# Kernel tuning notes

Hardware: AMD Instinct MI355X
Metric: run time of the kernel (lower is better)

The kernel has to match this reference:

```python
import jax, jax.numpy as jnp
import numpy as np

N, F_IN, H, E, G = 100000, 128, 64, 1600000, 256
BN_EPS = 1e-5


def setup_inputs() -> dict:
    key = jax.random.key(0)
    ks = jax.random.split(key, 32)
    rn = lambda k, shp, s=0.1: jax.random.normal(k, shp, jnp.float32) * s
    ru = lambda k, shp: jax.random.uniform(k, shp, jnp.float32)
    inp = {
        'x': jax.random.normal(ks[0], (N, F_IN), jnp.float32),
        'edge_index': jax.random.randint(ks[1], (2, E), 0, N),
        'batch': jnp.sort(jax.random.randint(ks[2], (N,), 0, G)),
        'w0': rn(ks[3], (F_IN, H)), 'b0': rn(ks[4], (H,)),
        'w1': rn(ks[5], (H, H)), 'b1': rn(ks[6], (H,)),
        'w2': rn(ks[7], (H, H)), 'b2': rn(ks[8], (H,)),
        'g0': ru(ks[9], (H,)) + 0.5, 'beta0': rn(ks[10], (H,)),
        'm0': rn(ks[11], (H,)), 'v0': ru(ks[12], (H,)) + 0.5,
        'g1': ru(ks[13], (H,)) + 0.5, 'beta1': rn(ks[14], (H,)),
        'm1': rn(ks[15], (H,)), 'v1': ru(ks[16], (H,)) + 0.5,
        'g2': ru(ks[17], (H,)) + 0.5, 'beta2': rn(ks[18], (H,)),
        'm2': rn(ks[19], (H,)), 'v2': ru(ks[20], (H,)) + 0.5,
        'l1w': rn(ks[21], (H, H // 2)), 'l1b': rn(ks[22], (H // 2,)),
        'l2w': rn(ks[23], (H // 2, 2)), 'l2b': rn(ks[24], (2,)),
    }
    return inp


def reference(x, edge_index, batch, w0, b0, w1, b1, w2, b2,
              g0, beta0, m0, v0, g1, beta1, m1, v1, g2, beta2, m2, v2,
              l1w, l1b, l2w, l2b):
    n = x.shape[0]
    # GCN: add self-loops, symmetric normalization deg^{-1/2} A_hat deg^{-1/2}
    loop = jnp.arange(n)
    src = jnp.concatenate([edge_index[0], loop])
    dst = jnp.concatenate([edge_index[1], loop])
    deg = jax.ops.segment_sum(jnp.ones_like(src, dtype=x.dtype), dst, num_segments=n)
    dinv = jax.lax.rsqrt(jnp.maximum(deg, 1.0))  # deg >= 1 after self-loops
    norm = (dinv[src] * dinv[dst])[:, None]      # [E+N, 1]

    def gcn(h, w, b):
        h = h @ w                                              # [N, H]
        agg = jax.ops.segment_sum(h[src] * norm, dst, num_segments=n)
        return agg + b

    def bn(h, g, be, m, v):  # eval-mode BatchNorm1d (running stats)
        return (h - m) * (g * jax.lax.rsqrt(v + BN_EPS)) + be

    h = jax.nn.relu(bn(gcn(x, w0, b0), g0, beta0, m0, v0))
    h = jax.nn.relu(bn(gcn(h, w1, b1), g1, beta1, m1, v1))
    h = jax.nn.relu(bn(gcn(h, w2, b2), g2, beta2, m2, v2))
    pooled = jax.ops.segment_sum(h, batch, num_segments=G)     # global_add_pool
    h = jax.nn.relu(pooled @ l1w + l1b)
    return h @ l2w + l2b                                        # [G, 2]
```

## Files before the change

### kernel.cpp

```cpp
#include <hip/hip_runtime.h>
#include <hip/hip_bf16.h>

#define BN_EPS 1e-5f

typedef short bf16x8 __attribute__((ext_vector_type(8)));
typedef float f32x4 __attribute__((ext_vector_type(4)));

static __device__ __forceinline__ unsigned short f2bf(float f) {
    unsigned u = __float_as_uint(f);
    unsigned r = (u + 0x7FFF + ((u >> 16) & 1)) >> 16;
    return (unsigned short)r;
}
static __device__ __forceinline__ float bf2f(unsigned short s) {
    return __uint_as_float((unsigned)s << 16);
}
__device__ __forceinline__ int pad4i(int c) { return (c + 3) & ~3; }

#define BIN_SHIFT 9
#define BIN_NODES 512
#define P1_CHUNK 8192
#define P1_THREADS 1024
#define P1_PER_THREAD (P1_CHUNK / P1_THREADS)
#define IMG_CAP 12288
#define P2_THREADS 512

__global__ __launch_bounds__(P1_THREADS) void phase1_kernel(
        const int* __restrict__ src, const int* __restrict__ dst,
        int* __restrict__ bincur, int* __restrict__ ebuf, int e, int ecap) {
    __shared__ int hist[256], base[256], cur[256];
    int t = threadIdx.x;
    int c0 = blockIdx.x * P1_CHUNK;
    int iend = c0 + P1_CHUNK; if (iend > e) iend = e;
    if (t < 256) hist[t] = 0;
    __syncthreads();
    int dreg[P1_PER_THREAD];
#pragma unroll
    for (int u = 0; u < P1_PER_THREAD; u++) {
        int i = c0 + t + u * P1_THREADS;
        if (i < iend) {
            int d = dst[i];
            dreg[u] = d;
            atomicAdd(&hist[d >> BIN_SHIFT], 1);
        }
    }
    __syncthreads();
    if (t < 256) {
        if (hist[t] > 0)
            base[t] = t * ecap + atomicAdd(&bincur[t], hist[t]);
        cur[t] = 0;
    }
    __syncthreads();
#pragma unroll
    for (int u = 0; u < P1_PER_THREAD; u++) {
        int i = c0 + t + u * P1_THREADS;
        if (i < iend) {
            int s = src[i], d = dreg[u];
            int b = d >> BIN_SHIFT;
            int r = atomicAdd(&cur[b], 1);
            int p = base[b] + r;
            if (p < (b + 1) * ecap)
                ebuf[p] = s | ((d & (BIN_NODES - 1)) << 17);
        }
    }
}

__global__ __launch_bounds__(1024) void bincount_kernel(
        const int* __restrict__ ebuf, const int* __restrict__ bincur, int ecap,
        float* __restrict__ dinv, int* __restrict__ row_start,
        int* __restrict__ row_len, int* __restrict__ binbase,
        int* __restrict__ binpad, int* __restrict__ gtotal,
        unsigned short* __restrict__ ha_sent, int n) {
    __shared__ int c512[BIN_NODES];
    __shared__ int sd[256];
    __shared__ int rbs;
    int b = blockIdx.x, t = threadIdx.x;
    if (b == 0 && t < 64) ha_sent[t] = 0;
    if (t < BIN_NODES) c512[t] = 0;
    __syncthreads();
    int cnt_b = bincur[b]; if (cnt_b > ecap) cnt_b = ecap;
    int e0 = b * ecap, e1 = e0 + cnt_b;
    for (int j = e0 + t; j < e1; j += 1024)
        atomicAdd(&c512[ebuf[j] >> 17], 1);
    __syncthreads();
    int n0 = b * BIN_NODES;
    if (t < BIN_NODES) {
        int i = n0 + t;
        if (i < n) dinv[i] = rsqrtf((float)(c512[t] + 1));
    }
    int v0 = 0, v1 = 0, tsum = 0;
    if (t < 256) {
        v0 = pad4i(c512[2 * t]);
        v1 = pad4i(c512[2 * t + 1]);
        tsum = v0 + v1;
        sd[t] = tsum;
    }
    __syncthreads();
    for (int off = 1; off < 256; off <<= 1) {
        int x = 0;
        if (t < 256 && t >= off) x = sd[t - off];
        __syncthreads();
        if (t < 256) sd[t] += x;
        __syncthreads();
    }
    if (t == 0) {
        int tot = sd[255];
        int rb = atomicAdd(gtotal, tot);
        rbs = rb; binbase[b] = rb; binpad[b] = tot;
    }
    __syncthreads();
    if (t < 256) {
        int rb = rbs;
        int excl = sd[t] - tsum;
        int i0 = n0 + 2 * t, i1 = i0 + 1;
        if (i0 < n) { row_start[i0] = rb + excl;      row_len[i0] = v0; }
        if (i1 < n) { row_start[i1] = rb + excl + v0; row_len[i1] = v1; }
    }
}

__global__ __launch_bounds__(P2_THREADS) void phase2_kernel(
        const int* __restrict__ ebuf, const int* __restrict__ bincur, int ecap,
        const int* __restrict__ row_start, const int* __restrict__ row_len,
        const int* __restrict__ binbase, const int* __restrict__ binpad,
        int* __restrict__ csr, int* __restrict__ gcursor, int n, int sentinel) {
    __shared__ int image[IMG_CAP];
    __shared__ int lcur[BIN_NODES];
    __shared__ int rl[BIN_NODES];
    int b = blockIdx.x, t = threadIdx.x;
    int n0 = b * BIN_NODES;
    int nloc = n - n0; if (nloc > BIN_NODES) nloc = BIN_NODES;
    int rb = binbase[b];
    int rspan = binpad[b];
    int cnt_b = bincur[b]; if (cnt_b > ecap) cnt_b = ecap;
    int e0 = b * ecap, e1 = e0 + cnt_b;
    if (t < BIN_NODES) {
        rl[t] = (t < nloc) ? row_start[n0 + t] - rb : 0;
        lcur[t] = 0;
    }
    __syncthreads();
    if (rspan <= IMG_CAP) {
        for (int k = t; k < rspan; k += P2_THREADS) image[k] = sentinel;
        __syncthreads();
        for (int j = e0 + t; j < e1; j += P2_THREADS) {
            int en = ebuf[j];
            int s = en & 0x1FFFF;
            int dl = en >> 17;
            int pos = rl[dl] + atomicAdd(&lcur[dl], 1);
            image[pos] = s;
        }
        __syncthreads();
        for (int k = t; k < rspan; k += P2_THREADS) csr[rb + k] = image[k];
    } else {
        for (int k = t; k < nloc; k += P2_THREADS) gcursor[n0 + k] = 0;
        __syncthreads();
        for (int j = e0 + t; j < e1; j += P2_THREADS) {
            int en = ebuf[j];
            int s = en & 0x1FFFF;
            int dl = en >> 17;
            int pos = rb + rl[dl] + atomicAdd(&gcursor[n0 + dl], 1);
            csr[pos] = s;
        }
        __syncthreads();
        for (int k = t; k < nloc; k += P2_THREADS) {
            int node = n0 + k;
            int st = rb + rl[k] + gcursor[node];
            int en2 = rb + rl[k] + row_len[node];
            for (int pos = st; pos < en2; pos++) csr[pos] = sentinel;
        }
    }
}

template<int K, bool BF16IN>
__global__ __launch_bounds__(256) void lin_mfma(const void* __restrict__ in_,
                                                const float* __restrict__ w,
                                                const float* __restrict__ dinv,
                                                unsigned short* __restrict__ outbf, int n) {
    constexpr int XS = K + 8;
    __shared__ unsigned short xs[64 * XS];
    __shared__ unsigned short wt[64 * XS];
    int t = threadIdx.x;
    int row0 = blockIdx.x * 64;
    int nrows = n - row0; if (nrows > 64) nrows = 64;

    {
        const float4* w4 = (const float4*)w;
        for (int idx = t; idx < K * 16; idx += 256) {
            int k = idx >> 4, c4 = (idx & 15) * 4;
            float4 v = w4[idx];
            wt[(c4 + 0) * XS + k] = f2bf(v.x);
            wt[(c4 + 1) * XS + k] = f2bf(v.y);
            wt[(c4 + 2) * XS + k] = f2bf(v.z);
            wt[(c4 + 3) * XS + k] = f2bf(v.w);
        }
    }
    if constexpr (BF16IN) {
        const uint4* in4 = (const uint4*)((const unsigned short*)in_ + (size_t)row0 * K);
        int total8 = nrows * (K / 8);
        for (int idx = t; idx < total8; idx += 256) {
            int r = idx / (K / 8), kk = idx - r * (K / 8);
            uint4 v = in4[idx];
            *(uint4*)&xs[r * XS + kk * 8] = v;
        }
    } else {
        const float4* in4 = (const float4*)((const float*)in_ + (size_t)row0 * K);
        int total4 = nrows * (K / 4);
        for (int idx = t; idx < total4; idx += 256) {
            int r = idx / (K / 4), kk = idx - r * (K / 4);
            float4 v = in4[idx];
            ushort4 s4;
            s4.x = f2bf(v.x); s4.y = f2bf(v.y); s4.z = f2bf(v.z); s4.w = f2bf(v.w);
            *(ushort4*)&xs[r * XS + kk * 4] = s4;
        }
    }
    __syncthreads();

    int lane = t & 63;
    int wid = t >> 6;
    int quad = lane >> 4;
    int l15 = lane & 15;

    f32x4 acc[4];
#pragma unroll
    for (int cg_ = 0; cg_ < 4; cg_++) acc[cg_] = (f32x4){0.f, 0.f, 0.f, 0.f};

    const unsigned short* xrow = &xs[(wid * 16 + l15) * XS + quad * 8];
#pragma unroll
    for (int kc = 0; kc < K / 32; kc++) {
        bf16x8 bfrag = *(const bf16x8*)(xrow + kc * 32);
#pragma unroll
        for (int cg_ = 0; cg_ < 4; cg_++) {
            bf16x8 afrag = *(const bf16x8*)&wt[(cg_ * 16 + l15) * XS + kc * 32 + quad * 8];
            acc[cg_] = __builtin_amdgcn_mfma_f32_16x16x32_bf16(afrag, bfrag, acc[cg_], 0, 0, 0);
        }
    }

    int grow = row0 + wid * 16 + l15;
    if (grow < n) {
        float dv = dinv[grow];
#pragma unroll
        for (int cg_ = 0; cg_ < 4; cg_++) {
            ushort4 st;
            st.x = f2bf(acc[cg_][0] * dv);
            st.y = f2bf(acc[cg_][1] * dv);
            st.z = f2bf(acc[cg_][2] * dv);
            st.w = f2bf(acc[cg_][3] * dv);
            *(ushort4*)&outbf[(size_t)grow * 64 + cg_ * 16 + quad * 4] = st;
        }
    }
}

template<bool POOL>
__global__ __launch_bounds__(256) void agg_kernel(
        const unsigned short* __restrict__ hs, const int* __restrict__ row_start,
        const int* __restrict__ row_len, const int* __restrict__ csr,
        const float* __restrict__ dinv,
        const float* __restrict__ bias, const float* __restrict__ gam,
        const float* __restrict__ bet, const float* __restrict__ mu,
        const float* __restrict__ var,
        unsigned short* __restrict__ out,
        const int* __restrict__ batch, float* __restrict__ pooled, int n) {
    int iw = blockIdx.x * 4 + (threadIdx.x >> 6);
    unsigned lane = threadIdx.x & 63;
    if (iw >= n) return;
    int i = __builtin_amdgcn_readfirstlane(iw);
    float acc = bf2f(hs[((unsigned)i << 6) + lane]);
    int rs = __builtin_amdgcn_readfirstlane(row_start[i]);
    int re = rs + __builtin_amdgcn_readfirstlane(row_len[i]);
    int j = rs;
    for (; j + 16 <= re; j += 16) {
        int s0 = __builtin_amdgcn_readfirstlane(csr[j + 0]);
        int s1 = __builtin_amdgcn_readfirstlane(csr[j + 1]);
        int s2 = __builtin_amdgcn_readfirstlane(csr[j + 2]);
        int s3 = __builtin_amdgcn_readfirstlane(csr[j + 3]);
        int s4 = __builtin_amdgcn_readfirstlane(csr[j + 4]);
        int s5 = __builtin_amdgcn_readfirstlane(csr[j + 5]);
        int s6 = __builtin_amdgcn_readfirstlane(csr[j + 6]);
        int s7 = __builtin_amdgcn_readfirstlane(csr[j + 7]);
        int s8 = __builtin_amdgcn_readfirstlane(csr[j + 8]);
        int s9 = __builtin_amdgcn_readfirstlane(csr[j + 9]);
        int sA = __builtin_amdgcn_readfirstlane(csr[j + 10]);
        int sB = __builtin_amdgcn_readfirstlane(csr[j + 11]);
        int sC = __builtin_amdgcn_readfirstlane(csr[j + 12]);
        int sD = __builtin_amdgcn_readfirstlane(csr[j + 13]);
        int sE = __builtin_amdgcn_readfirstlane(csr[j + 14]);
        int sF = __builtin_amdgcn_readfirstlane(csr[j + 15]);
        float h0 = bf2f(hs[((unsigned)s0 << 6) + lane]);
        float h1 = bf2f(hs[((unsigned)s1 << 6) + lane]);
        float h2 = bf2f(hs[((unsigned)s2 << 6) + lane]);
        float h3 = bf2f(hs[((unsigned)s3 << 6) + lane]);
        float h4 = bf2f(hs[((unsigned)s4 << 6) + lane]);
        float h5 = bf2f(hs[((unsigned)s5 << 6) + lane]);
        float h6 = bf2f(hs[((unsigned)s6 << 6) + lane]);
        float h7 = bf2f(hs[((unsigned)s7 << 6) + lane]);
        float h8 = bf2f(hs[((unsigned)s8 << 6) + lane]);
        float h9 = bf2f(hs[((unsigned)s9 << 6) + lane]);
        float hA = bf2f(hs[((unsigned)sA << 6) + lane]);
        float hB = bf2f(hs[((unsigned)sB << 6) + lane]);
        float hC = bf2f(hs[((unsigned)sC << 6) + lane]);
        float hD = bf2f(hs[((unsigned)sD << 6) + lane]);
        float hE = bf2f(hs[((unsigned)sE << 6) + lane]);
        float hF = bf2f(hs[((unsigned)sF << 6) + lane]);
        acc += (((h0 + h1) + (h2 + h3)) + ((h4 + h5) + (h6 + h7)))
             + (((h8 + h9) + (hA + hB)) + ((hC + hD) + (hE + hF)));
    }
    for (; j < re; j += 4) {
        int s0 = __builtin_amdgcn_readfirstlane(csr[j + 0]);
        int s1 = __builtin_amdgcn_readfirstlane(csr[j + 1]);
        int s2 = __builtin_amdgcn_readfirstlane(csr[j + 2]);
        int s3 = __builtin_amdgcn_readfirstlane(csr[j + 3]);
        float h0 = bf2f(hs[((unsigned)s0 << 6) + lane]);
        float h1 = bf2f(hs[((unsigned)s1 << 6) + lane]);
        float h2 = bf2f(hs[((unsigned)s2 << 6) + lane]);
        float h3 = bf2f(hs[((unsigned)s3 << 6) + lane]);
        acc += (h0 + h1) + (h2 + h3);
    }
    float agg = acc * dinv[i];
    float scale = gam[lane] * rsqrtf(var[lane] + BN_EPS);
    float r = (agg + bias[lane] - mu[lane]) * scale + bet[lane];
    unsigned short sv = f2bf(r > 0.f ? r : 0.f);
    out[((unsigned)i << 6) + lane] = sv;
    if (POOL) {
        int g = __builtin_amdgcn_readfirstlane(batch[i]);
        atomicAdd(&pooled[(size_t)g * 64 + lane], bf2f(sv));
    }
}

__global__ void mlp_kernel(const float* __restrict__ pooled,
                           const float* __restrict__ l1w, const float* __restrict__ l1b,
                           const float* __restrict__ l2w, const float* __restrict__ l2b,
                           float* __restrict__ out) {
    int g = blockIdx.x;
    int lane = threadIdx.x;
    __shared__ float p[64];
    __shared__ float h1[32];
    p[lane] = pooled[(size_t)g * 64 + lane];
    __syncthreads();
    if (lane < 32) {
        float a = l1b[lane];
#pragma unroll 8
        for (int k = 0; k < 64; k++) a += p[k] * l1w[k * 32 + lane];
        h1[lane] = a > 0.f ? a : 0.f;
    }
    __syncthreads();
    if (lane < 2) {
        float a = l2b[lane];
#pragma unroll 8
        for (int j = 0; j < 32; j++) a += h1[j] * l2w[j * 2 + lane];
        out[g * 2 + lane] = a;
    }
}

extern "C" void kernel_launch(void* const* d_in, const int* in_sizes, int n_in,
                              void* d_out, int out_size, void* d_ws, size_t ws_size,
                              hipStream_t stream) {
    const float* x     = (const float*)d_in[0];
    const int*   ei    = (const int*)d_in[1];
    const int*   batch = (const int*)d_in[2];
    const float* w0 = (const float*)d_in[3];
    const float* b0 = (const float*)d_in[4];
    const float* w1 = (const float*)d_in[5];
    const float* b1 = (const float*)d_in[6];
    const float* w2 = (const float*)d_in[7];
    const float* b2 = (const float*)d_in[8];
    const float* g0 = (const float*)d_in[9];
    const float* be0 = (const float*)d_in[10];
    const float* m0 = (const float*)d_in[11];
    const float* v0 = (const float*)d_in[12];
    const float* g1 = (const float*)d_in[13];
    const float* be1 = (const float*)d_in[14];
    const float* m1 = (const float*)d_in[15];
    const float* v1 = (const float*)d_in[16];
    const float* g2 = (const float*)d_in[17];
    const float* be2 = (const float*)d_in[18];
    const float* m2 = (const float*)d_in[19];
    const float* v2 = (const float*)d_in[20];
    const float* l1w = (const float*)d_in[21];
    const float* l1b = (const float*)d_in[22];
    const float* l2w = (const float*)d_in[23];
    const float* l2b = (const float*)d_in[24];
    float* out = (float*)d_out;

    const int N = in_sizes[2];
    const int E = in_sizes[1] / 2;
    const int G = out_size / 2;
    const int NBINS = (N + BIN_NODES - 1) / BIN_NODES;
    int ECAP = ((2 * (E / NBINS)) + 1023) & ~1023;
    if (ECAP < 2048) ECAP = 2048;

    const int* src = ei;
    const int* dst = ei + E;

    char* p = (char*)d_ws;
    auto alloc = [&](size_t bytes) -> void* {
        void* r = (void*)p;
        p += (bytes + 255) & ~(size_t)255;
        return r;
    };
    const size_t CSR_CAP = (size_t)E + 4 * (size_t)N + 64;
    float* dinvp    = (float*)alloc((size_t)N * 4);
    int*   row_start= (int*)alloc((size_t)N * 4);
    int*   row_len  = (int*)alloc((size_t)N * 4);
    int*   gcursor  = (int*)alloc((size_t)N * 4);
    int*   binbase  = (int*)alloc((size_t)NBINS * 4);
    int*   binpad   = (int*)alloc((size_t)NBINS * 4);
    int*   bincur   = (int*)alloc((size_t)NBINS * 4);
    int*   gtotal   = (int*)alloc(4);
    float* pooled   = (float*)alloc((size_t)G * 64 * 4);
    char*  zero_end = p;
    int*   ebuf     = (int*)alloc((size_t)NBINS * ECAP * 4);
    int*   csr      = (int*)alloc(CSR_CAP * 4);
    unsigned short* h_a = (unsigned short*)alloc((size_t)(N + 1) * 64 * 2);
    unsigned short* h_b = (unsigned short*)alloc((size_t)N * 64 * 2);
    (void)ws_size;

    hipMemsetAsync(bincur, 0, (size_t)(zero_end - (char*)bincur), stream);
    const int nchunks = (E + P1_CHUNK - 1) / P1_CHUNK;
    phase1_kernel<<<nchunks, P1_THREADS, 0, stream>>>(src, dst, bincur, ebuf, E, ECAP);
    bincount_kernel<<<NBINS, 1024, 0, stream>>>(ebuf, bincur, ECAP, dinvp,
                                                row_start, row_len, binbase,
                                                binpad, gtotal,
                                                h_a + (size_t)N * 64, N);
    phase2_kernel<<<NBINS, P2_THREADS, 0, stream>>>(ebuf, bincur, ECAP, row_start,
                                                    row_len, binbase, binpad,
                                                    csr, gcursor, N, N);

    const int nblk = (N + 3) / 4;
    const int lblk = (N + 63) / 64;
    lin_mfma<128, false><<<lblk, 256, 0, stream>>>(x, w0, dinvp, h_a, N);
    agg_kernel<false><<<nblk, 256, 0, stream>>>(h_a, row_start, row_len, csr, dinvp,
                                                b0, g0, be0, m0, v0, h_b,
                                                batch, pooled, N);
    lin_mfma<64, true><<<lblk, 256, 0, stream>>>(h_b, w1, dinvp, h_a, N);
    agg_kernel<false><<<nblk, 256, 0, stream>>>(h_a, row_start, row_len, csr, dinvp,
                                                b1, g1, be1, m1, v1, h_b,
                                                batch, pooled, N);
    lin_mfma<64, true><<<lblk, 256, 0, stream>>>(h_b, w2, dinvp, h_a, N);
    agg_kernel<true><<<nblk, 256, 0, stream>>>(h_a, row_start, row_len, csr, dinvp,
                                               b2, g2, be2, m2, v2, h_b,
                                               batch, pooled, N);
    mlp_kernel<<<G, 64, 0, stream>>>(pooled, l1w, l1b, l2w, l2b, out);
}
```

Measured before the change: 347.5 us.

## Fuse bin count and CSR scatter kernels, vectorize edge loads in binning

Merges the per-bin degree counting/prefix-scan kernel and the CSR image scatter kernel into one build kernel, so bin bases and offsets stay in shared memory instead of going through global binbase/binpad/row_start arrays and a second pass over ebuf. Phase1 now uses smaller 512-thread blocks with 4096-edge chunks and int4 vector loads for full aligned chunks. The build kernel reads ebuf with int4 loads and does a 512-wide scan. The aim is to remove one launch and redundant global traffic. The cost is a larger shared-memory footprint per block, which may lower occupancy.

```diff
diff --git a/kernel.cpp b/kernel.cpp
--- a/kernel.cpp
+++ b/kernel.cpp
@@ -18,11 +18,10 @@
 
 #define BIN_SHIFT 9
 #define BIN_NODES 512
-#define P1_CHUNK 8192
-#define P1_THREADS 1024
-#define P1_PER_THREAD (P1_CHUNK / P1_THREADS)
+#define P1_CHUNK 4096
+#define P1_THREADS 512
 #define IMG_CAP 12288
-#define P2_THREADS 512
+#define BUILD_THREADS 512
 
 __global__ __launch_bounds__(P1_THREADS) void phase1_kernel(
         const int* __restrict__ src, const int* __restrict__ dst,
@@ -30,142 +29,158 @@
     __shared__ int hist[256], base[256], cur[256];
     int t = threadIdx.x;
     int c0 = blockIdx.x * P1_CHUNK;
-    int iend = c0 + P1_CHUNK; if (iend > e) iend = e;
-    if (t < 256) hist[t] = 0;
-    __syncthreads();
-    int dreg[P1_PER_THREAD];
-#pragma unroll
-    for (int u = 0; u < P1_PER_THREAD; u++) {
-        int i = c0 + t + u * P1_THREADS;
-        if (i < iend) {
-            int d = dst[i];
-            dreg[u] = d;
-            atomicAdd(&hist[d >> BIN_SHIFT], 1);
-        }
-    }
-    __syncthreads();
-    if (t < 256) {
-        if (hist[t] > 0)
-            base[t] = t * ecap + atomicAdd(&bincur[t], hist[t]);
-        cur[t] = 0;
-    }
-    __syncthreads();
-#pragma unroll
-    for (int u = 0; u < P1_PER_THREAD; u++) {
-        int i = c0 + t + u * P1_THREADS;
-        if (i < iend) {
-            int s = src[i], d = dreg[u];
-            int b = d >> BIN_SHIFT;
-            int r = atomicAdd(&cur[b], 1);
-            int p = base[b] + r;
-            if (p < (b + 1) * ecap)
-                ebuf[p] = s | ((d & (BIN_NODES - 1)) << 17);
-        }
-    }
-}
-
-__global__ __launch_bounds__(1024) void bincount_kernel(
+    if (t < 256) { hist[t] = 0; }
+    __syncthreads();
+    bool full = (c0 + P1_CHUNK <= e) &&
+                (((((unsigned long long)(const void*)dst) |
+                   ((unsigned long long)(const void*)src)) & 15ull) == 0ull);
+    if (full) {
+        const int4* d4 = (const int4*)(dst + c0);
+        int4 da = d4[t], db = d4[t + P1_THREADS];
+        atomicAdd(&hist[da.x >> BIN_SHIFT], 1);
+        atomicAdd(&hist[da.y >> BIN_SHIFT], 1);
+        atomicAdd(&hist[da.z >> BIN_SHIFT], 1);
+        atomicAdd(&hist[da.w >> BIN_SHIFT], 1);
+        atomicAdd(&hist[db.x >> BIN_SHIFT], 1);
+        atomicAdd(&hist[db.y >> BIN_SHIFT], 1);
+        atomicAdd(&hist[db.z >> BIN_SHIFT], 1);
+        atomicAdd(&hist[db.w >> BIN_SHIFT], 1);
+        __syncthreads();
+        if (t < 256) {
+            if (hist[t] > 0)
+                base[t] = t * ecap + atomicAdd(&bincur[t], hist[t]);
+            cur[t] = 0;
+        }
+        __syncthreads();
+        const int4* s4 = (const int4*)(src + c0);
+        int4 sa = s4[t], sb = s4[t + P1_THREADS];
+#define P1_SCAT(D, S)                                                         \
+        {                                                                     \
+            int b_ = (D) >> BIN_SHIFT;                                        \
+            int r_ = atomicAdd(&cur[b_], 1);                                  \
+            int p_ = base[b_] + r_;                                           \
+            if (p_ < (b_ + 1) * ecap)                                         \
+                ebuf[p_] = (S) | (((D) & (BIN_NODES - 1)) << 17);             \
+        }
+        P1_SCAT(da.x, sa.x) P1_SCAT(da.y, sa.y) P1_SCAT(da.z, sa.z) P1_SCAT(da.w, sa.w)
+        P1_SCAT(db.x, sb.x) P1_SCAT(db.y, sb.y) P1_SCAT(db.z, sb.z) P1_SCAT(db.w, sb.w)
+    } else {
+        int iend = c0 + P1_CHUNK; if (iend > e) iend = e;
+        int dreg[8];
+#pragma unroll
+        for (int u = 0; u < 8; u++) {
+            int i = c0 + t + u * P1_THREADS;
+            if (i < iend) {
+                int d = dst[i];
+                dreg[u] = d;
+                atomicAdd(&hist[d >> BIN_SHIFT], 1);
+            }
+        }
+        __syncthreads();
+        if (t < 256) {
+            if (hist[t] > 0)
+                base[t] = t * ecap + atomicAdd(&bincur[t], hist[t]);
+            cur[t] = 0;
+        }
+        __syncthreads();
+#pragma unroll
+        for (int u = 0; u < 8; u++) {
+            int i = c0 + t + u * P1_THREADS;
+            if (i < iend) {
+                int s = src[i], d = dreg[u];
+                P1_SCAT(d, s)
+            }
+        }
+#undef P1_SCAT
+    }
+}
+
+__global__ __launch_bounds__(BUILD_THREADS) void build_kernel(
         const int* __restrict__ ebuf, const int* __restrict__ bincur, int ecap,
         float* __restrict__ dinv, int* __restrict__ row_start,
-        int* __restrict__ row_len, int* __restrict__ binbase,
-        int* __restrict__ binpad, int* __restrict__ gtotal,
-        unsigned short* __restrict__ ha_sent, int n) {
+        int* __restrict__ row_len, int* __restrict__ gtotal,
+        int* __restrict__ csr, int* __restrict__ gcursor,
+        unsigned short* __restrict__ ha_sent, int n, int sentinel) {
+    __shared__ int image[IMG_CAP];
     __shared__ int c512[BIN_NODES];
-    __shared__ int sd[256];
+    __shared__ int sd[BIN_NODES];
+    __shared__ int rl[BIN_NODES];
+    __shared__ int lcur[BIN_NODES];
     __shared__ int rbs;
     int b = blockIdx.x, t = threadIdx.x;
     if (b == 0 && t < 64) ha_sent[t] = 0;
-    if (t < BIN_NODES) c512[t] = 0;
+    c512[t] = 0;
+    lcur[t] = 0;
     __syncthreads();
     int cnt_b = bincur[b]; if (cnt_b > ecap) cnt_b = ecap;
-    int e0 = b * ecap, e1 = e0 + cnt_b;
-    for (int j = e0 + t; j < e1; j += 1024)
-        atomicAdd(&c512[ebuf[j] >> 17], 1);
+    int e0 = b * ecap;
+    int cnt4 = cnt_b >> 2, rem = cnt_b & 3;
+    const int4* eb4 = (const int4*)(ebuf + e0);
+    for (int j = t; j < cnt4; j += BUILD_THREADS) {
+        int4 v = eb4[j];
+        atomicAdd(&c512[v.x >> 17], 1);
+        atomicAdd(&c512[v.y >> 17], 1);
+        atomicAdd(&c512[v.z >> 17], 1);
+        atomicAdd(&c512[v.w >> 17], 1);
+    }
+    if (t < rem) atomicAdd(&c512[ebuf[e0 + cnt4 * 4 + t] >> 17], 1);
     __syncthreads();
     int n0 = b * BIN_NODES;
-    if (t < BIN_NODES) {
-        int i = n0 + t;
-        if (i < n) dinv[i] = rsqrtf((float)(c512[t] + 1));
-    }
-    int v0 = 0, v1 = 0, tsum = 0;
-    if (t < 256) {
-        v0 = pad4i(c512[2 * t]);
-        v1 = pad4i(c512[2 * t + 1]);
-        tsum = v0 + v1;
-        sd[t] = tsum;
-    }
-    __syncthreads();
-    for (int off = 1; off < 256; off <<= 1) {
-        int x = 0;
-        if (t < 256 && t >= off) x = sd[t - off];
-        __syncthreads();
-        if (t < 256) sd[t] += x;
-        __syncthreads();
-    }
-    if (t == 0) {
-        int tot = sd[255];
-        int rb = atomicAdd(gtotal, tot);
-        rbs = rb; binbase[b] = rb; binpad[b] = tot;
-    }
-    __syncthreads();
-    if (t < 256) {
-        int rb = rbs;
-        int excl = sd[t] - tsum;
-        int i0 = n0 + 2 * t, i1 = i0 + 1;
-        if (i0 < n) { row_start[i0] = rb + excl;      row_len[i0] = v0; }
-        if (i1 < n) { row_start[i1] = rb + excl + v0; row_len[i1] = v1; }
-    }
-}
-
-__global__ __launch_bounds__(P2_THREADS) void phase2_kernel(
-        const int* __restrict__ ebuf, const int* __restrict__ bincur, int ecap,
-        const int* __restrict__ row_start, const int* __restrict__ row_len,
-        const int* __restrict__ binbase, const int* __restrict__ binpad,
-        int* __restrict__ csr, int* __restrict__ gcursor, int n, int sentinel) {
-    __shared__ int image[IMG_CAP];
-    __shared__ int lcur[BIN_NODES];
-    __shared__ int rl[BIN_NODES];
-    int b = blockIdx.x, t = threadIdx.x;
-    int n0 = b * BIN_NODES;
-    int nloc = n - n0; if (nloc > BIN_NODES) nloc = BIN_NODES;
-    int rb = binbase[b];
-    int rspan = binpad[b];
-    int cnt_b = bincur[b]; if (cnt_b > ecap) cnt_b = ecap;
-    int e0 = b * ecap, e1 = e0 + cnt_b;
-    if (t < BIN_NODES) {
-        rl[t] = (t < nloc) ? row_start[n0 + t] - rb : 0;
-        lcur[t] = 0;
-    }
-    __syncthreads();
+    int deg = c512[t];
+    if (n0 + t < n) dinv[n0 + t] = rsqrtf((float)(deg + 1));
+    int pv = pad4i(deg);
+    sd[t] = pv;
+    __syncthreads();
+    for (int off = 1; off < BIN_NODES; off <<= 1) {
+        int x = (t >= off) ? sd[t - off] : 0;
+        __syncthreads();
+        sd[t] += x;
+        __syncthreads();
+    }
+    int excl = sd[t] - pv;
+    rl[t] = excl;
+    if (t == BIN_NODES - 1) rbs = atomicAdd(gtotal, sd[BIN_NODES - 1]);
+    __syncthreads();
+    int rb = rbs;
+    int rspan = sd[BIN_NODES - 1];
+    if (n0 + t < n) {
+        row_start[n0 + t] = rb + excl;
+        row_len[n0 + t] = pv;
+    }
     if (rspan <= IMG_CAP) {
-        for (int k = t; k < rspan; k += P2_THREADS) image[k] = sentinel;
-        __syncthreads();
-        for (int j = e0 + t; j < e1; j += P2_THREADS) {
-            int en = ebuf[j];
-            int s = en & 0x1FFFF;
-            int dl = en >> 17;
-            int pos = rl[dl] + atomicAdd(&lcur[dl], 1);
-            image[pos] = s;
-        }
-        __syncthreads();
-        for (int k = t; k < rspan; k += P2_THREADS) csr[rb + k] = image[k];
+        for (int k = t; k < rspan; k += BUILD_THREADS) image[k] = sentinel;
+        __syncthreads();
+        for (int j = t; j < cnt4; j += BUILD_THREADS) {
+            int4 v = eb4[j];
+#define B_SCAT(EN)                                                            \
+            {                                                                 \
+                int dl_ = (EN) >> 17;                                         \
+                int pos_ = rl[dl_] + atomicAdd(&lcur[dl_], 1);                \
+                image[pos_] = (EN) & 0x1FFFF;                                 \
+            }
+            B_SCAT(v.x) B_SCAT(v.y) B_SCAT(v.z) B_SCAT(v.w)
+        }
+        if (t < rem) { int en = ebuf[e0 + cnt4 * 4 + t]; B_SCAT(en) }
+        __syncthreads();
+        for (int k = t; k < rspan; k += BUILD_THREADS) csr[rb + k] = image[k];
     } else {
-        for (int k = t; k < nloc; k += P2_THREADS) gcursor[n0 + k] = 0;
-        __syncthreads();
-        for (int j = e0 + t; j < e1; j += P2_THREADS) {
-            int en = ebuf[j];
+        int nloc = n - n0; if (nloc > BIN_NODES) nloc = BIN_NODES;
+        if (t < nloc) gcursor[n0 + t] = 0;
+        __syncthreads();
+        for (int j = t; j < cnt_b; j += BUILD_THREADS) {
+            int en = ebuf[e0 + j];
             int s = en & 0x1FFFF;
             int dl = en >> 17;
             int pos = rb + rl[dl] + atomicAdd(&gcursor[n0 + dl], 1);
             csr[pos] = s;
         }
         __syncthreads();
-        for (int k = t; k < nloc; k += P2_THREADS) {
-            int node = n0 + k;
-            int st = rb + rl[k] + gcursor[node];
-            int en2 = rb + rl[k] + row_len[node];
+        if (t < nloc) {
+            int st = rb + rl[t] + gcursor[n0 + t];
+            int en2 = rb + rl[t] + pv;
             for (int pos = st; pos < en2; pos++) csr[pos] = sentinel;
         }
+#undef B_SCAT
     }
 }
 
@@ -400,8 +415,6 @@
     int*   row_start= (int*)alloc((size_t)N * 4);
     int*   row_len  = (int*)alloc((size_t)N * 4);
     int*   gcursor  = (int*)alloc((size_t)N * 4);
-    int*   binbase  = (int*)alloc((size_t)NBINS * 4);
-    int*   binpad   = (int*)alloc((size_t)NBINS * 4);
     int*   bincur   = (int*)alloc((size_t)NBINS * 4);
     int*   gtotal   = (int*)alloc(4);
     float* pooled   = (float*)alloc((size_t)G * 64 * 4);
@@ -415,13 +428,10 @@
     hipMemsetAsync(bincur, 0, (size_t)(zero_end - (char*)bincur), stream);
     const int nchunks = (E + P1_CHUNK - 1) / P1_CHUNK;
     phase1_kernel<<<nchunks, P1_THREADS, 0, stream>>>(src, dst, bincur, ebuf, E, ECAP);
-    bincount_kernel<<<NBINS, 1024, 0, stream>>>(ebuf, bincur, ECAP, dinvp,
-                                                row_start, row_len, binbase,
-                                                binpad, gtotal,
-                                                h_a + (size_t)N * 64, N);
-    phase2_kernel<<<NBINS, P2_THREADS, 0, stream>>>(ebuf, bincur, ECAP, row_start,
-                                                    row_len, binbase, binpad,
-                                                    csr, gcursor, N, N);
+    build_kernel<<<NBINS, BUILD_THREADS, 0, stream>>>(ebuf, bincur, ECAP, dinvp,
+                                                      row_start, row_len, gtotal,
+                                                      csr, gcursor,
+                                                      h_a + (size_t)N * 64, N, N);
 
     const int nblk = (N + 3) / 4;
     const int lblk = (N + 63) / 64;
```

Result: no change. 350.3 us (+0.8%).
